# Optimization experiments

Measured on AMD Instinct MI355X. Metric: run time of the kernel, lower is better.

## Reference

```python
import jax, jax.numpy as jnp
import numpy as np

C_M, C_Z, C_H = 256, 128, 32
EPS = 1e-3
LN_EPS = 1e-5


def setup_inputs() -> dict:
    key = jax.random.key(0)
    ks = jax.random.split(key, 10)
    S, R = 128, 256
    inp = {
        'm_1': jax.random.normal(ks[0], (S, R, C_M), jnp.float32),
        'm_2': jax.random.normal(ks[1], (S, R, C_M), jnp.float32),
        'mask_1': jnp.ones((S, R), jnp.float32),
        'mask_2': jnp.ones((S, R), jnp.float32),
        # LayerNorm params
        'ln1_w': jnp.ones((C_M,), jnp.float32),
        'ln1_b': jnp.zeros((C_M,), jnp.float32),
        'ln2_w': jnp.ones((C_M,), jnp.float32),
        'ln2_b': jnp.zeros((C_M,), jnp.float32),
        # Linear params
        'w1': jax.random.normal(ks[2], (C_M, C_H), jnp.float32) * (1.0 / np.sqrt(C_M)),
        'b1': jnp.zeros((C_H,), jnp.float32),
        'w2': jax.random.normal(ks[3], (C_M, C_H), jnp.float32) * (1.0 / np.sqrt(C_M)),
        'b2': jnp.zeros((C_H,), jnp.float32),
        'w_out': jax.random.normal(ks[4], (C_H * C_H, C_Z), jnp.float32) * 0.02,
        'b_out': jnp.zeros((C_Z,), jnp.float32),
    }
    return inp


def _layer_norm(x, w, b):
    mu = jnp.mean(x, axis=-1, keepdims=True)
    var = jnp.mean(jnp.square(x - mu), axis=-1, keepdims=True)
    return (x - mu) * jax.lax.rsqrt(var + LN_EPS) * w + b


def reference(m_1, m_2, mask_1, mask_2, ln1_w, ln1_b, ln2_w, ln2_b,
              w1, b1, w2, b2, w_out, b_out):
    # m_*: [S, R, C_M]; mask_*: [S, R]
    a = (_layer_norm(m_1, ln1_w, ln1_b) @ w1 + b1) * mask_1[..., None]  # [S,R,H]
    b = (_layer_norm(m_2, ln2_w, ln2_b) @ w2 + b2) * mask_2[..., None]  # [S,R,H]
    # outer product mean over sequence dim: [R, R, H, H]
    outer = jnp.einsum('sic,sje->ijce', a, b)
    S, R, H = a.shape
    outer = outer.reshape(R, R, H * H)
    z = outer @ w_out + b_out  # [R, R, C_Z]
    norm = jnp.einsum('si,sj->ij', mask_1, mask_2)[..., None] + EPS  # [R,R,1]
    return z / norm
```

## Files before the change

kernel.cpp:

```cpp
#include <hip/hip_runtime.h>
#include <hip/hip_bf16.h>

#define S_DIM 128
#define R_DIM 256
#define CM    256
#define H_DIM 32
#define CZ    128

typedef short s8v   __attribute__((ext_vector_type(8)));
typedef float f32x4 __attribute__((ext_vector_type(4)));
typedef float f32x16 __attribute__((ext_vector_type(16)));
using bf16 = __hip_bfloat16;

static __device__ __forceinline__ unsigned short bf16_bits(float f) {
  return __builtin_bit_cast(unsigned short, __float2bfloat16(f));
}

static __device__ __forceinline__ void gload_lds16(const void* g, void* l) {
  __builtin_amdgcn_global_load_lds(
      (const __attribute__((address_space(1))) unsigned int*)g,
      (__attribute__((address_space(3))) unsigned int*)l, 16, 0, 0);
}

__global__ __launch_bounds__(256) void opm_prep(
    const float* __restrict__ w_out,
    const float* __restrict__ mask1, const float* __restrict__ mask2,
    const float* __restrict__ w1, const float* __restrict__ w2,
    bf16* __restrict__ wT2, float* __restrict__ rnorm, bf16* __restrict__ wF)
{
  const int b   = blockIdx.x;
  const int tid = threadIdx.x;
  if (b < 64) {
    const int vid  = b*256 + tid;
    const int lane = vid & 63;
    const int ks2  = (vid >> 6) & 63;
    const int tb   = vid >> 12;
    const int t    = tb*32 + (lane & 31);
    const int hf   = lane >> 5;
    unsigned int pk[4];
    #pragma unroll
    for (int ep = 0; ep < 4; ++ep) {
      const int ce0 = ks2*16 + hf*8 + ep*2;
      const int ce1 = ce0 + 1;
      unsigned int w0 = bf16_bits(w_out[((ce0 & 31)*32 + (ce0 >> 5))*CZ + t]);
      unsigned int w1b = bf16_bits(w_out[((ce1 & 31)*32 + (ce1 >> 5))*CZ + t]);
      pk[ep] = w0 | (w1b << 16);
    }
    uint4 o = {pk[0], pk[1], pk[2], pk[3]};
    *reinterpret_cast<uint4*>((char*)wT2 + (size_t)vid*16) = o;
  } else if (b < 320) {
    const int i = b - 64;
    const int j = tid;
    float acc = 0.f;
    for (int s = 0; s < S_DIM; ++s)
      acc += mask1[(size_t)s*R_DIM + i] * mask2[(size_t)s*R_DIM + j];
    rnorm[i*R_DIM + j] = 1.0f / (acc + 1e-3f);
  } else {
    const int mat = b - 320;
    const float* __restrict__ w = mat ? w2 : w1;
    bf16* __restrict__ dst = wF + mat*8192;
    #pragma unroll
    for (int it = 0; it < 4; ++it) {
      const int vid  = it*256 + tid;
      const int nf   = vid >> 9;
      const int ks   = (vid >> 6) & 7;
      const int lane = vid & 63;
      const int h    = nf*16 + (lane & 15);
      unsigned int pk[4];
      #pragma unroll
      for (int ep = 0; ep < 4; ++ep) {
        const int c0 = ks*32 + (lane >> 4)*8 + ep*2;
        unsigned int lo = bf16_bits(w[c0*H_DIM + h]);
        unsigned int hi = bf16_bits(w[(c0 + 1)*H_DIM + h]);
        pk[ep] = lo | (hi << 16);
      }
      uint4 o = {pk[0], pk[1], pk[2], pk[3]};
      *reinterpret_cast<uint4*>((char*)dst + (size_t)vid*16) = o;
    }
  }
}

__global__ __launch_bounds__(64) void opm_proj(
    const float* __restrict__ m1, const float* __restrict__ m2,
    const float* __restrict__ ln1w, const float* __restrict__ ln1b,
    const float* __restrict__ ln2w, const float* __restrict__ ln2b,
    const float* __restrict__ b1, const float* __restrict__ b2,
    const float* __restrict__ mask1, const float* __restrict__ mask2,
    const bf16* __restrict__ wF, bf16* __restrict__ aT, bf16* __restrict__ bT)
{
  __shared__ char xn[8192];

  const int mat = blockIdx.y;
  const float* __restrict__ m    = mat ? m2   : m1;
  const float* __restrict__ lnw  = mat ? ln2w : ln1w;
  const float* __restrict__ lnb  = mat ? ln2b : ln1b;
  const float* __restrict__ bias = mat ? b2   : b1;
  const float* __restrict__ mask = mat ? mask2 : mask1;
  const bf16* __restrict__ wf    = wF + mat*8192;
  bf16* __restrict__ dst         = mat ? bT   : aT;

  const int lane = threadIdx.x;
  const int g16  = lane >> 4;
  const int c16  = lane & 15;
  const int r    = blockIdx.x & 255;
  const int sb   = blockIdx.x >> 8;

  float4 x[4][4];
  #pragma unroll
  for (int p = 0; p < 4; ++p) {
    const int s = sb*16 + p*4 + g16;
    const float4* __restrict__ src =
        reinterpret_cast<const float4*>(m + ((size_t)s*R_DIM + r)*CM);
    #pragma unroll
    for (int it = 0; it < 4; ++it)
      x[p][it] = src[c16 + it*16];
  }
  const float4* __restrict__ lnw4 = reinterpret_cast<const float4*>(lnw);
  const float4* __restrict__ lnb4 = reinterpret_cast<const float4*>(lnb);
  float4 lw[4], lb[4];
  #pragma unroll
  for (int it = 0; it < 4; ++it) {
    lw[it] = lnw4[c16 + it*16];
    lb[it] = lnb4[c16 + it*16];
  }
  float mk[4];
  #pragma unroll
  for (int rr = 0; rr < 4; ++rr)
    mk[rr] = mask[(size_t)(sb*16 + g16*4 + rr)*R_DIM + r];
  const float bv0 = bias[c16];
  const float bv1 = bias[16 + c16];

  float sum[4], sq[4];
  #pragma unroll
  for (int p = 0; p < 4; ++p) {
    float s0 = 0.f, s1 = 0.f;
    #pragma unroll
    for (int it = 0; it < 4; ++it) {
      const float4 v = x[p][it];
      s0 += v.x + v.y + v.z + v.w;
      s1 += v.x*v.x + v.y*v.y + v.z*v.z + v.w*v.w;
    }
    sum[p] = s0; sq[p] = s1;
  }
  #pragma unroll
  for (int off = 1; off < 16; off <<= 1) {
    #pragma unroll
    for (int p = 0; p < 4; ++p) {
      sum[p] += __shfl_xor(sum[p], off);
      sq[p]  += __shfl_xor(sq[p], off);
    }
  }
  float mu[4], rs[4];
  #pragma unroll
  for (int p = 0; p < 4; ++p) {
    mu[p] = sum[p] * (1.0f/CM);
    rs[p] = rsqrtf(sq[p] * (1.0f/CM) - mu[p]*mu[p] + 1e-5f);
  }

  #pragma unroll
  for (int p = 0; p < 4; ++p) {
    const int row = p*4 + g16;
    #pragma unroll
    for (int it = 0; it < 4; ++it) {
      const float v0 = (x[p][it].x - mu[p])*rs[p]*lw[it].x + lb[it].x;
      const float v1 = (x[p][it].y - mu[p])*rs[p]*lw[it].y + lb[it].y;
      const float v2 = (x[p][it].z - mu[p])*rs[p]*lw[it].z + lb[it].z;
      const float v3 = (x[p][it].w - mu[p])*rs[p]*lw[it].w + lb[it].w;
      uint2 pk;
      pk.x = (unsigned)bf16_bits(v0) | ((unsigned)bf16_bits(v1) << 16);
      pk.y = (unsigned)bf16_bits(v2) | ((unsigned)bf16_bits(v3) << 16);
      int off = row*512 + c16*8 + it*128;
      off ^= (row & 7) << 4;
      *reinterpret_cast<uint2*>(xn + off) = pk;
    }
  }
  __syncthreads();

  const int row = c16;
  const int q   = g16;
  f32x4 z0 = {bv0, bv0, bv0, bv0};
  f32x4 z1 = {bv1, bv1, bv1, bv1};
  #pragma unroll
  for (int ks = 0; ks < 8; ++ks) {
    int off = row*512 + ks*64 + q*16;
    off ^= (row & 7) << 4;
    const s8v a  = *reinterpret_cast<const s8v*>(xn + off);
    const s8v w0 = *reinterpret_cast<const s8v*>((const char*)wf + (ks*64 + lane)*16);
    const s8v w1 = *reinterpret_cast<const s8v*>((const char*)wf + ((8 + ks)*64 + lane)*16);
    z0 = __builtin_amdgcn_mfma_f32_16x16x32_bf16(a, w0, z0, 0, 0, 0);
    z1 = __builtin_amdgcn_mfma_f32_16x16x32_bf16(a, w1, z1, 0, 0, 0);
  }

  unsigned int pa0 = (unsigned)bf16_bits(z0[0]*mk[0]) | ((unsigned)bf16_bits(z0[1]*mk[1]) << 16);
  unsigned int pa1 = (unsigned)bf16_bits(z0[2]*mk[2]) | ((unsigned)bf16_bits(z0[3]*mk[3]) << 16);
  unsigned int pb0 = (unsigned)bf16_bits(z1[0]*mk[0]) | ((unsigned)bf16_bits(z1[1]*mk[1]) << 16);
  unsigned int pb1 = (unsigned)bf16_bits(z1[2]*mk[2]) | ((unsigned)bf16_bits(z1[3]*mk[3]) << 16);

  const int p0 = r*H_DIM + row;
  const int p1 = r*H_DIM + 16 + row;
  const int c0 = sb*2 + (q >> 1);
  const int rem = (q & 1) * 8;
  {
    uint2 v; v.x = pa0; v.y = pa1;
    *reinterpret_cast<uint2*>((char*)dst + (size_t)p0*256 + ((c0 ^ (p0 & 15)) << 4) + rem) = v;
  }
  {
    uint2 v; v.x = pb0; v.y = pb1;
    *reinterpret_cast<uint2*>((char*)dst + (size_t)p1*256 + ((c0 ^ (p1 & 15)) << 4) + rem) = v;
  }
}

__global__ __launch_bounds__(1024, 4) void opm_gemm(
    const bf16* __restrict__ aT, const bf16* __restrict__ bT,
    const bf16* __restrict__ wT2, const float* __restrict__ b_out,
    const float* __restrict__ rnorm, float* __restrict__ out)
{
  __shared__ char smem[131072];

  const int tid  = threadIdx.x;
  const int lane = tid & 63;
  const int wid  = tid >> 6;
  const int l31  = lane & 31;
  const int hf   = lane >> 5;

  int swz = blockIdx.x;
  swz = (swz & 7)*128 + (swz >> 3);
  const int bx = swz >> 5, by = swz & 31;

  {
    const char* gA = (const char*)aT + (size_t)bx*65536;
    const char* gB = (const char*)bT + (size_t)by*65536;
    #pragma unroll
    for (int i = 0; i < 4; ++i) {
      const int base = (i*16 + wid)*1024;
      gload_lds16(gA + base + lane*16, smem + base);
      gload_lds16(gB + base + lane*16, smem + 65536 + base);
    }
  }
  __syncthreads();

  const int wm = wid >> 2, wn = wid & 3;
  f32x16 acc[2][2];
  #pragma unroll
  for (int mf = 0; mf < 2; ++mf)
    #pragma unroll
    for (int nf = 0; nf < 2; ++nf)
      #pragma unroll
      for (int r = 0; r < 16; ++r) acc[mf][nf][r] = 0.f;

  #pragma unroll
  for (int ks = 0; ks < 8; ++ks) {
    s8v af[2], bfv[2];
    #pragma unroll
    for (int mf = 0; mf < 2; ++mf) {
      const int mm = wm*64 + mf*32 + l31;
      int L = (mm*256 + ks*32 + hf*16) ^ ((mm & 15) << 4);
      af[mf] = *reinterpret_cast<const s8v*>(smem + L);
    }
    #pragma unroll
    for (int nf = 0; nf < 2; ++nf) {
      const int nn = wn*64 + nf*32 + l31;
      int L = (nn*256 + ks*32 + hf*16) ^ ((nn & 15) << 4);
      bfv[nf] = *reinterpret_cast<const s8v*>(smem + 65536 + L);
    }
    #pragma unroll
    for (int mf = 0; mf < 2; ++mf)
      #pragma unroll
      for (int nf = 0; nf < 2; ++nf)
        acc[mf][nf] = __builtin_amdgcn_mfma_f32_32x32x16_bf16(af[mf], bfv[nf], acc[mf][nf], 0, 0, 0);
  }
  __syncthreads();

  #pragma unroll
  for (int mf = 0; mf < 2; ++mf) {
    #pragma unroll
    for (int nf = 0; nf < 2; ++nf) {
      const int pair = (wm*2 + mf)*8 + wn*2 + nf;
      #pragma unroll
      for (int g = 0; g < 4; ++g) {
        const unsigned int lo = (unsigned)bf16_bits(acc[mf][nf][4*g+0]) |
                                ((unsigned)bf16_bits(acc[mf][nf][4*g+1]) << 16);
        const unsigned int hi = (unsigned)bf16_bits(acc[mf][nf][4*g+2]) |
                                ((unsigned)bf16_bits(acc[mf][nf][4*g+3]) << 16);
        const int L0 = pair*2048 + (l31*32 + 8*g + 4*hf)*2;
        const int L  = L0 ^ ((((pair & 15) ^ ((L0 >> 7) & 15))) << 4);
        uint2 v; v.x = lo; v.y = hi;
        *reinterpret_cast<uint2*>(smem + L) = v;
      }
    }
  }
  __syncthreads();

  const int kq = wm, pn = wn;
  const char* wb = (const char*)wT2 + ((size_t)(pn*64 + kq*16)*64 + lane)*16;
  s8v bwr[16];
  #pragma unroll
  for (int i = 0; i < 16; ++i)
    bwr[i] = *reinterpret_cast<const s8v*>(wb + i*1024);

  const int t = pn*32 + l31;
  f32x16 z0, z1;
  {
    const float init = (kq == 0) ? b_out[t] : 0.f;
    #pragma unroll
    for (int r = 0; r < 16; ++r) { z0[r] = init; z1[r] = init; }
  }
  #pragma unroll
  for (int ks = 0; ks < 16; ++ks) {
    const int ks2 = kq*16 + ks;
    {
      const int pair = l31;
      int L0 = pair*2048 + ks2*32 + hf*16;
      int L  = L0 ^ ((((pair & 15) ^ ((L0 >> 7) & 15))) << 4);
      const s8v a = *reinterpret_cast<const s8v*>(smem + L);
      z0 = __builtin_amdgcn_mfma_f32_32x32x16_bf16(a, bwr[ks], z0, 0, 0, 0);
    }
    {
      const int pair = 32 + l31;
      int L0 = pair*2048 + ks2*32 + hf*16;
      int L  = L0 ^ ((((pair & 15) ^ ((L0 >> 7) & 15))) << 4);
      const s8v a = *reinterpret_cast<const s8v*>(smem + L);
      z1 = __builtin_amdgcn_mfma_f32_32x32x16_bf16(a, bwr[ks], z1, 0, 0, 0);
    }
  }
  __syncthreads();

  {
    const int base = wid*8192;
    #pragma unroll
    for (int g = 0; g < 4; ++g) {
      f32x4 v0 = {z0[4*g+0], z0[4*g+1], z0[4*g+2], z0[4*g+3]};
      f32x4 v1 = {z1[4*g+0], z1[4*g+1], z1[4*g+2], z1[4*g+3]};
      *reinterpret_cast<f32x4*>(smem + base +        g*1024 + lane*16) = v0;
      *reinterpret_cast<f32x4*>(smem + base + 4096 + g*1024 + lane*16) = v1;
    }
  }
  __syncthreads();

  {
    const int chain = kq & 1;
    const int gh    = kq >> 1;
    f32x4 f[2];
    #pragma unroll
    for (int gg = 0; gg < 2; ++gg) {
      const int g = gh*2 + gg;
      f32x4 s = {0.f, 0.f, 0.f, 0.f};
      #pragma unroll
      for (int kk = 0; kk < 4; ++kk) {
        const int base = (kk*4 + pn)*8192 + chain*4096;
        const f32x4 p = *reinterpret_cast<const f32x4*>(smem + base + g*1024 + lane*16);
        #pragma unroll
        for (int j = 0; j < 4; ++j) s[j] += p[j];
      }
      f[gg] = s;
    }
    #pragma unroll
    for (int gg = 0; gg < 2; ++gg) {
      const int g = gh*2 + gg;
      #pragma unroll
      for (int j = 0; j < 4; ++j) {
        const int row  = j + 4*hf + 8*g;
        const int pair = chain*32 + row;
        const int o    = (bx*8 + (pair >> 3))*R_DIM + by*8 + (pair & 7);
        out[(size_t)o*CZ + t] = f[gg][j] * rnorm[o];
      }
    }
  }
}

extern "C" void kernel_launch(void* const* d_in, const int* in_sizes, int n_in,
                              void* d_out, int out_size, void* d_ws, size_t ws_size,
                              hipStream_t stream) {
  const float* m_1    = (const float*)d_in[0];
  const float* m_2    = (const float*)d_in[1];
  const float* mask_1 = (const float*)d_in[2];
  const float* mask_2 = (const float*)d_in[3];
  const float* ln1_w  = (const float*)d_in[4];
  const float* ln1_b  = (const float*)d_in[5];
  const float* ln2_w  = (const float*)d_in[6];
  const float* ln2_b  = (const float*)d_in[7];
  const float* w1     = (const float*)d_in[8];
  const float* b1     = (const float*)d_in[9];
  const float* w2     = (const float*)d_in[10];
  const float* b2     = (const float*)d_in[11];
  const float* w_out  = (const float*)d_in[12];
  const float* b_out  = (const float*)d_in[13];
  float* out = (float*)d_out;

  char* ws = (char*)d_ws;
  bf16* aT    = (bf16*)ws;
  bf16* bT    = (bf16*)(ws + (2u << 20));
  bf16* wT2   = (bf16*)(ws + (4u << 20));
  float* rnrm = (float*)(ws + (4u << 20) + (256u << 10));
  bf16* wF    = (bf16*)(ws + (4u << 20) + (512u << 10));

  opm_prep<<<dim3(322),      dim3(256), 0, stream>>>(w_out, mask_1, mask_2,
      w1, w2, wT2, rnrm, wF);
  opm_proj<<<dim3(2048, 2),  dim3(64),  0, stream>>>(m_1, m_2, ln1_w, ln1_b,
      ln2_w, ln2_b, b1, b2, mask_1, mask_2, wF, aT, bT);
  opm_gemm<<<dim3(1024),     dim3(1024), 0, stream>>>(aT, bT, wT2, b_out, rnrm, out);
}
```

Before: 73.04 us.

## Replace split-K 32x32 output GEMM with full-K 16x16 MFMA tiles

The projection to C_Z used to split K across warps with 32x32x16 MFMAs, then reduce the partial sums through shared memory with two extra barriers. Now each warp owns a 16-pair by 32-channel output tile and runs the full K with 16x16x32 MFMAs, writing results directly. The prep kernel reorders w_out to match the new fragment layout. This removes the LDS reduction and its syncs. In exchange, w_out fragments are streamed from global memory inside the loop instead of being preloaded into registers, and the smaller MFMAs give less reuse per instruction.

```diff
diff --git a/kernel.cpp b/kernel.cpp
--- a/kernel.cpp
+++ b/kernel.cpp
@@ -33,18 +33,19 @@
   if (b < 64) {
     const int vid  = b*256 + tid;
     const int lane = vid & 63;
-    const int ks2  = (vid >> 6) & 63;
-    const int tb   = vid >> 12;
-    const int t    = tb*32 + (lane & 31);
-    const int hf   = lane >> 5;
+    const int vec  = vid >> 6;
+    const int tb16 = vec >> 5;
+    const int ks   = vec & 31;
+    const int q    = lane >> 4;
+    const int t    = tb16*16 + (lane & 15);
     unsigned int pk[4];
     #pragma unroll
     for (int ep = 0; ep < 4; ++ep) {
-      const int ce0 = ks2*16 + hf*8 + ep*2;
-      const int ce1 = ce0 + 1;
-      unsigned int w0 = bf16_bits(w_out[((ce0 & 31)*32 + (ce0 >> 5))*CZ + t]);
-      unsigned int w1b = bf16_bits(w_out[((ce1 & 31)*32 + (ce1 >> 5))*CZ + t]);
-      pk[ep] = w0 | (w1b << 16);
+      const int k0 = ks*32 + q*8 + ep*2;
+      const int k1 = k0 + 1;
+      unsigned int v0 = bf16_bits(w_out[((k0 & 31)*32 + (k0 >> 5))*CZ + t]);
+      unsigned int v1 = bf16_bits(w_out[((k1 & 31)*32 + (k1 >> 5))*CZ + t]);
+      pk[ep] = v0 | (v1 << 16);
     }
     uint4 o = {pk[0], pk[1], pk[2], pk[3]};
     *reinterpret_cast<uint4*>((char*)wT2 + (size_t)vid*16) = o;
@@ -291,79 +292,39 @@
   }
   __syncthreads();
 
-  const int kq = wm, pn = wn;
-  const char* wb = (const char*)wT2 + ((size_t)(pn*64 + kq*16)*64 + lane)*16;
-  s8v bwr[16];
-  #pragma unroll
-  for (int i = 0; i < 16; ++i)
-    bwr[i] = *reinterpret_cast<const s8v*>(wb + i*1024);
-
-  const int t = pn*32 + l31;
-  f32x16 z0, z1;
   {
-    const float init = (kq == 0) ? b_out[t] : 0.f;
-    #pragma unroll
-    for (int r = 0; r < 16; ++r) { z0[r] = init; z1[r] = init; }
-  }
-  #pragma unroll
-  for (int ks = 0; ks < 16; ++ks) {
-    const int ks2 = kq*16 + ks;
-    {
-      const int pair = l31;
-      int L0 = pair*2048 + ks2*32 + hf*16;
+    const int pm = wid >> 2, pn = wid & 3;
+    const int l15 = lane & 15;
+    const int q4  = lane >> 4;
+    const int tA  = pn*32 + l15;
+    const int tB  = tA + 16;
+    const float bo0 = b_out[tA];
+    const float bo1 = b_out[tB];
+    f32x4 z0 = {bo0, bo0, bo0, bo0};
+    f32x4 z1 = {bo1, bo1, bo1, bo1};
+
+    const int pair = pm*16 + l15;
+    const char* wb0 = (const char*)wT2 + (((size_t)(pn*2 + 0)*32)*64 + lane)*16;
+    const char* wb1 = (const char*)wT2 + (((size_t)(pn*2 + 1)*32)*64 + lane)*16;
+
+    #pragma unroll 8
+    for (int ks = 0; ks < 32; ++ks) {
+      int L0 = pair*2048 + ks*64 + q4*16;
       int L  = L0 ^ ((((pair & 15) ^ ((L0 >> 7) & 15))) << 4);
-      const s8v a = *reinterpret_cast<const s8v*>(smem + L);
-      z0 = __builtin_amdgcn_mfma_f32_32x32x16_bf16(a, bwr[ks], z0, 0, 0, 0);
-    }
-    {
-      const int pair = 32 + l31;
-      int L0 = pair*2048 + ks2*32 + hf*16;
-      int L  = L0 ^ ((((pair & 15) ^ ((L0 >> 7) & 15))) << 4);
-      const s8v a = *reinterpret_cast<const s8v*>(smem + L);
-      z1 = __builtin_amdgcn_mfma_f32_32x32x16_bf16(a, bwr[ks], z1, 0, 0, 0);
-    }
-  }
-  __syncthreads();
-
-  {
-    const int base = wid*8192;
-    #pragma unroll
-    for (int g = 0; g < 4; ++g) {
-      f32x4 v0 = {z0[4*g+0], z0[4*g+1], z0[4*g+2], z0[4*g+3]};
-      f32x4 v1 = {z1[4*g+0], z1[4*g+1], z1[4*g+2], z1[4*g+3]};
-      *reinterpret_cast<f32x4*>(smem + base +        g*1024 + lane*16) = v0;
-      *reinterpret_cast<f32x4*>(smem + base + 4096 + g*1024 + lane*16) = v1;
-    }
-  }
-  __syncthreads();
-
-  {
-    const int chain = kq & 1;
-    const int gh    = kq >> 1;
-    f32x4 f[2];
-    #pragma unroll
-    for (int gg = 0; gg < 2; ++gg) {
-      const int g = gh*2 + gg;
-      f32x4 s = {0.f, 0.f, 0.f, 0.f};
-      #pragma unroll
-      for (int kk = 0; kk < 4; ++kk) {
-        const int base = (kk*4 + pn)*8192 + chain*4096;
-        const f32x4 p = *reinterpret_cast<const f32x4*>(smem + base + g*1024 + lane*16);
-        #pragma unroll
-        for (int j = 0; j < 4; ++j) s[j] += p[j];
-      }
-      f[gg] = s;
-    }
-    #pragma unroll
-    for (int gg = 0; gg < 2; ++gg) {
-      const int g = gh*2 + gg;
-      #pragma unroll
-      for (int j = 0; j < 4; ++j) {
-        const int row  = j + 4*hf + 8*g;
-        const int pair = chain*32 + row;
-        const int o    = (bx*8 + (pair >> 3))*R_DIM + by*8 + (pair & 7);
-        out[(size_t)o*CZ + t] = f[gg][j] * rnorm[o];
-      }
+      const s8v a  = *reinterpret_cast<const s8v*>(smem + L);
+      const s8v w0 = *reinterpret_cast<const s8v*>(wb0 + ks*1024);
+      const s8v w1 = *reinterpret_cast<const s8v*>(wb1 + ks*1024);
+      z0 = __builtin_amdgcn_mfma_f32_16x16x32_bf16(a, w0, z0, 0, 0, 0);
+      z1 = __builtin_amdgcn_mfma_f32_16x16x32_bf16(a, w1, z1, 0, 0, 0);
+    }
+
+    #pragma unroll
+    for (int j = 0; j < 4; ++j) {
+      const int pr = pm*16 + q4*4 + j;
+      const int o  = (bx*8 + (pr >> 3))*R_DIM + by*8 + (pr & 7);
+      const float rn = rnorm[o];
+      out[(size_t)o*CZ + tA] = z0[j] * rn;
+      out[(size_t)o*CZ + tB] = z1[j] * rn;
     }
   }
 }
```

Measured after the change: 87.68 us. 20.0% more time.
